# Kernel optimization log

Hardware: AMD Instinct MI355X
Metric: run time of the kernel (lower is better)

Reference implementation:

```python
import jax, jax.numpy as jnp
import numpy as np

TOP_K = 2
SCALING = 32.0 / 64.0  # lora_alpha / reservoir_size


def setup_inputs() -> dict:
    key = jax.random.key(0)
    ks = jax.random.split(key, 6)
    Bsz, S, Din, Dout, R, E = 4, 2048, 4096, 4096, 64, 16
    x = jax.random.normal(ks[0], (Bsz, S, Din), dtype=jnp.float32)
    base_w = jax.random.normal(ks[1], (Dout, Din), dtype=jnp.float32) * 0.02
    base_b = jax.random.normal(ks[2], (Dout,), dtype=jnp.float32) * 0.02
    A = jax.random.normal(ks[3], (R, Din), dtype=jnp.float32) * (1.0 / np.sqrt(Din))
    B = jax.random.normal(ks[4], (E, Dout, R), dtype=jnp.float32) * 0.02
    router_w = jax.random.normal(ks[5], (E, Din), dtype=jnp.float32) * 0.02
    return {"x": x, "base_w": base_w, "base_b": base_b, "A": A, "B": B, "router_w": router_w}


def reference(x, base_w, base_b, A, B, router_w):
    # base linear: [b,s,din] @ [dout,din]^T + bias
    base_out = jnp.einsum('bsi,oi->bso', x, base_w) + base_b
    # low-rank projection through fixed reservoir A (activation=identity, dropout off)
    res_hidden = jnp.einsum('bsi,ri->bsr', x, A)          # [b,s,r]
    # routing
    logits = jnp.einsum('bsi,ei->bse', x, router_w)       # [b,s,E]
    probs = jax.nn.softmax(logits, axis=-1)
    topw, topi = jax.lax.top_k(probs, TOP_K)              # [b,s,k]
    topw = topw / (jnp.sum(topw, axis=-1, keepdims=True) + 1e-6)
    num_experts = B.shape[0]
    # combine weights per expert: sum_k w_k * onehot(idx_k)  -> [b,s,E]
    combine = jnp.sum(jax.nn.one_hot(topi, num_experts, dtype=x.dtype) * topw[..., None], axis=-2)
    # weighted per-expert lowrank B matmul and combine
    delta = jnp.einsum('bse,bsr,eor->bso', combine, res_hidden, B)
    return base_out + delta * SCALING
```

## Files before the change

### kernel.cpp

```cpp
#include <hip/hip_runtime.h>
#include <cstdint>
#include <cstddef>

typedef short short8 __attribute__((ext_vector_type(8)));
typedef float f32x4 __attribute__((ext_vector_type(4)));

#define DIN  4096
#define DOUT 4096
#define RANK 64
#define NEXP 16
#define NTOK 8192
#define KCAT 5120
#define NKT  (KCAT / 64)
#define ROWB (KCAT * 2)

__device__ __forceinline__ unsigned short f2bf(float f) {
    unsigned int u = __builtin_bit_cast(unsigned int, f);
    u = (u + 0x7FFFu + ((u >> 16) & 1u)) >> 16;
    return (unsigned short)u;
}
__device__ __forceinline__ void async_cp16(const void* g, void* lds) {
    __builtin_amdgcn_global_load_lds(
        (const __attribute__((address_space(1))) void*)g,
        (__attribute__((address_space(3))) void*)lds, 16, 0, 0);
}

__global__ void __launch_bounds__(256) prep_all_kernel(
        const float* __restrict__ x, const float* __restrict__ rw,
        const float* __restrict__ bw, const float* __restrict__ Bm,
        const float* __restrict__ Am,
        unsigned short* __restrict__ Xcat, unsigned short* __restrict__ Wcat,
        unsigned short* __restrict__ W1A, float* __restrict__ Lg) {
    __shared__ __align__(16) float xsl[8][532];
    __shared__ __align__(16) float red[8][16][16];
    const int tid = threadIdx.x;

    if (blockIdx.x < 1024) {
        const int t0 = blockIdx.x * 8;
        const int tt = tid >> 5, l32 = tid & 31;
        const int eg = tid >> 6, ts = (tid >> 4) & 3, cc = tid & 15;
        float part[2][4] = {};

        for (int w = 0; w < 8; ++w) {
            #pragma unroll
            for (int sub = 0; sub < 4; ++sub) {
                const int col = w * 512 + sub * 128 + l32 * 4;
                const float4 xv = *(const float4*)&x[(size_t)(t0 + tt) * DIN + col];
                unsigned short b0 = f2bf(xv.x), b1 = f2bf(xv.y),
                               b2 = f2bf(xv.z), b3 = f2bf(xv.w);
                uint2 pk = { (unsigned)b0 | ((unsigned)b1 << 16),
                             (unsigned)b2 | ((unsigned)b3 << 16) };
                *(uint2*)&Xcat[(size_t)(t0 + tt) * KCAT + col] = pk;
                *(float4*)&xsl[tt][sub * 128 + l32 * 4] = xv;
            }
            __syncthreads();
            #pragma unroll
            for (int j = 0; j < 8; ++j) {
                const int colb = w * 512 + (j * 16 + cc) * 4;
                const float4 r0 = *(const float4*)&rw[(size_t)(eg * 4 + 0) * DIN + colb];
                const float4 r1 = *(const float4*)&rw[(size_t)(eg * 4 + 1) * DIN + colb];
                const float4 r2 = *(const float4*)&rw[(size_t)(eg * 4 + 2) * DIN + colb];
                const float4 r3 = *(const float4*)&rw[(size_t)(eg * 4 + 3) * DIN + colb];
                #pragma unroll
                for (int t2 = 0; t2 < 2; ++t2) {
                    const int t = ts * 2 + t2;
                    const float4 xv = *(const float4*)&xsl[t][(j * 16 + cc) * 4];
                    part[t2][0] += xv.x * r0.x + xv.y * r0.y + xv.z * r0.z + xv.w * r0.w;
                    part[t2][1] += xv.x * r1.x + xv.y * r1.y + xv.z * r1.z + xv.w * r1.w;
                    part[t2][2] += xv.x * r2.x + xv.y * r2.y + xv.z * r2.z + xv.w * r2.w;
                    part[t2][3] += xv.x * r3.x + xv.y * r3.y + xv.z * r3.z + xv.w * r3.w;
                }
            }
            __syncthreads();
        }
        #pragma unroll
        for (int t2 = 0; t2 < 2; ++t2)
            #pragma unroll
            for (int e = 0; e < 4; ++e)
                red[ts * 2 + t2][eg * 4 + e][cc] = part[t2][e];
        __syncthreads();
        if (tid < 128) {
            const int t = tid >> 4, e = tid & 15;
            float s = 0.f;
            #pragma unroll
            for (int c = 0; c < 16; ++c) s += red[t][e][c];
            Lg[(size_t)(t0 + t) * NEXP + e] = s;
        }
    } else {
        const unsigned NG1 = (unsigned)DOUT * KCAT / 8u;
        const unsigned NGT = NG1 + 64u * DIN / 8u;
        for (unsigned g = (blockIdx.x - 1024) * 256u + tid; g < NGT;
             g += 2048u * 256u) {
            const float* src;
            unsigned short* dst;
            if (g < NG1) {
                unsigned o  = g / 640u;
                unsigned c8 = (g - o * 640u) * 8u;
                dst = Wcat + (size_t)o * KCAT + c8;
                if (c8 < DIN) {
                    src = bw + (size_t)o * DIN + c8;
                } else {
                    unsigned cc2 = c8 - DIN;
                    unsigned e = cc2 >> 6, r = cc2 & 63u;
                    src = Bm + ((size_t)e * DOUT + o) * RANK + r;
                }
            } else {
                unsigned g2 = g - NG1;
                unsigned row = g2 >> 9;
                unsigned c8  = (g2 & 511u) * 8u;
                dst = W1A + (size_t)row * DIN + c8;
                src = Am + (size_t)row * DIN + c8;
            }
            float4 v0 = *(const float4*)(src);
            float4 v1 = *(const float4*)(src + 4);
            uint4 pk;
            pk.x = (unsigned)f2bf(v0.x) | ((unsigned)f2bf(v0.y) << 16);
            pk.y = (unsigned)f2bf(v0.z) | ((unsigned)f2bf(v0.w) << 16);
            pk.z = (unsigned)f2bf(v1.x) | ((unsigned)f2bf(v1.y) << 16);
            pk.w = (unsigned)f2bf(v1.z) | ((unsigned)f2bf(v1.w) << 16);
            *(uint4*)dst = pk;
        }
    }
}

__global__ void __launch_bounds__(256) proj_moe_kernel(
        const unsigned short* __restrict__ Xcat,
        const unsigned short* __restrict__ W1A,
        const float* __restrict__ Lg, unsigned short* __restrict__ XcatW) {
    __shared__ __align__(16) unsigned short Xs[16 * 128];
    __shared__ __align__(16) unsigned short Ws[64 * 128];
    __shared__ __align__(16) float cw[16][16];
    __shared__ __align__(16) float hbuf[16][68];
    const int tid = threadIdx.x;
    const int wave = tid >> 6, lane = tid & 63;
    const int quad = lane >> 4, l16 = lane & 15;
    const int t0 = blockIdx.x * 16;

    const int rX = tid >> 4, cXs = tid & 15;
    const int cX = (cXs & 8) | ((cXs ^ rX) & 7);

    if (tid < 16) {
        float l[16];
        #pragma unroll
        for (int e = 0; e < 16; ++e) l[e] = Lg[(size_t)(t0 + tid) * NEXP + e];
        int i1 = 0; float b1v = l[0];
        #pragma unroll
        for (int e = 1; e < 16; ++e) if (l[e] > b1v) { b1v = l[e]; i1 = e; }
        int i2 = -1; float b2v = -1e30f;
        #pragma unroll
        for (int e = 0; e < 16; ++e) if (e != i1 && l[e] > b2v) { b2v = l[e]; i2 = e; }
        float S = 0.f;
        #pragma unroll
        for (int e = 0; e < 16; ++e) S += expf(l[e] - b1v);
        const float p1 = 1.0f / S;
        const float p2 = expf(b2v - b1v) / S;
        const float d = p1 + p2 + 1e-6f;
        const float c1 = 0.5f * p1 / d;
        const float c2 = 0.5f * p2 / d;
        #pragma unroll
        for (int e = 0; e < 16; ++e)
            cw[tid][e] = (e == i1) ? c1 : (e == i2) ? c2 : 0.0f;
    }

    f32x4 acc = {};
    for (int kt = 0; kt < DIN / 128; ++kt) {
        const int k0 = kt * 128;
        async_cp16(Xcat + (size_t)(t0 + rX) * KCAT + k0 + cX * 8,
                   (char*)Xs + wave * 1024);
        #pragma unroll
        for (int i = 0; i < 4; ++i) {
            const int s = i * 256 + tid;
            const int rW = s >> 4, cWs = s & 15;
            const int cWc = (cWs & 8) | ((cWs ^ rW) & 7);
            async_cp16(W1A + (size_t)rW * DIN + k0 + cWc * 8,
                       (char*)Ws + i * 4096 + wave * 1024);
        }
        __syncthreads();
        #pragma unroll
        for (int kk = 0; kk < 4; ++kk) {
            const int c = kk * 4 + quad;
            const int sa = ((c & 8) | ((c ^ l16) & 7)) << 3;
            const int rb = wave * 16 + l16;
            const int sb = ((c & 8) | ((c ^ rb) & 7)) << 3;
            short8 am = *(const short8*)&Xs[l16 * 128 + sa];
            short8 bn = *(const short8*)&Ws[rb * 128 + sb];
            acc = __builtin_amdgcn_mfma_f32_16x16x32_bf16(am, bn, acc, 0, 0, 0);
        }
        __syncthreads();
    }
    #pragma unroll
    for (int r = 0; r < 4; ++r)
        hbuf[quad * 4 + r][wave * 16 + l16] = acc[r];
    __syncthreads();
    const int t = tid >> 4, e = tid & 15;
    const float c = cw[t][e];
    unsigned short* dst = XcatW + (size_t)(t0 + t) * KCAT + DIN + e * 64;
    #pragma unroll
    for (int r8 = 0; r8 < 8; ++r8) {
        unsigned short o16[8];
        #pragma unroll
        for (int k = 0; k < 8; ++k)
            o16[k] = f2bf(c * hbuf[t][r8 * 8 + k]);
        uint4 pk;
        pk.x = (unsigned)o16[0] | ((unsigned)o16[1] << 16);
        pk.y = (unsigned)o16[2] | ((unsigned)o16[3] << 16);
        pk.z = (unsigned)o16[4] | ((unsigned)o16[5] << 16);
        pk.w = (unsigned)o16[6] | ((unsigned)o16[7] << 16);
        *(uint4*)(dst + r8 * 8) = pk;
    }
}

__global__ void __launch_bounds__(512, 2) gemm_main_kernel(
        const unsigned short* __restrict__ Xcat,
        const unsigned short* __restrict__ Wcat,
        const float* __restrict__ bias, float* __restrict__ out) {
    __shared__ __align__(16) unsigned short As[2][256 * 64];
    __shared__ __align__(16) unsigned short Bs[2][256 * 64];

    const int tid  = threadIdx.x;
    const int wave = tid >> 6, lane = tid & 63;
    const int l16  = lane & 15, quad = lane >> 4, xb = l16 & 7;
    const int wm   = wave >> 2, wn = wave & 3;

    const int bid = blockIdx.x;
    const int swz = (bid & 7) * 64 + (bid >> 3);
    const int bm0 = (swz & 31) * 256;
    const int bn0 = (swz >> 5) * 256;

    const int urr = tid >> 3;
    const int cks = (tid & 7) ^ (urr & 7);
    const unsigned voffG = (unsigned)(urr * KCAT + cks * 8) * 2u;

    const char* gA = (const char*)Xcat + (size_t)bm0 * ROWB + voffG;
    const char* gB = (const char*)Wcat + (size_t)bn0 * ROWB + voffG;
    char* const ldsA  = (char*)&As[0][0];
    char* const ldsB  = (char*)&Bs[0][0];
    char* const ldswA = ldsA + wave * 1024;
    char* const ldswB = ldsB + wave * 1024;

#define STAGE_A(H, TT, BOFF2) { \
    async_cp16(gA + (size_t)((H) * 64) * ROWB + (size_t)(TT) * 128, \
               ldswA + (BOFF2) + (H) * 8192); \
    async_cp16(gA + (size_t)((H) * 64 + 128) * ROWB + (size_t)(TT) * 128, \
               ldswA + (BOFF2) + (H) * 8192 + 16384); }
#define STAGE_B(U, TT, BOFF2) { \
    async_cp16(gB + (size_t)((U) * 128) * ROWB + (size_t)(TT) * 128, \
               ldswB + (BOFF2) + (U) * 16384); \
    async_cp16(gB + (size_t)((U) * 128 + 64) * ROWB + (size_t)(TT) * 128, \
               ldswB + (BOFF2) + (U) * 16384 + 8192); }

    const int kof0 = ((quad)     ^ xb) * 16;
    const int kof1 = ((4 + quad) ^ xb) * 16;
    const char* ldsAw = ldsA + wm * 16384 + l16 * 128;
    const char* ldsBw = ldsB + wn * 8192  + l16 * 128;

    f32x4 acc[8][4] = {};
    short8 bf[8];
    short8 fE[4], fO[4];

#define READ_BF(BOFF2) { \
    _Pragma("unroll") \
    for (int n = 0; n < 4; ++n) { \
        bf[n * 2 + 0] = *(const short8*)(ldsBw + (BOFF2) + n * 2048 + kof0); \
        bf[n * 2 + 1] = *(const short8*)(ldsBw + (BOFF2) + n * 2048 + kof1); \
    } }
#define PREF_A(DST, Q, BOFF2) { \
    _Pragma("unroll") \
    for (int mm = 0; mm < 2; ++mm) { \
        DST[mm * 2 + 0] = *(const short8*)(ldsAw + (BOFF2) + (2 * (Q) + mm) * 2048 + kof0); \
        DST[mm * 2 + 1] = *(const short8*)(ldsAw + (BOFF2) + (2 * (Q) + mm) * 2048 + kof1); \
    } }
#define MFMA16(AF, Q) { \
    __builtin_amdgcn_s_setprio(1); \
    _Pragma("unroll") \
    for (int kk = 0; kk < 2; ++kk) \
        _Pragma("unroll") \
        for (int mm = 0; mm < 2; ++mm) \
            _Pragma("unroll") \
            for (int n = 0; n < 4; ++n) \
                acc[2 * (Q) + mm][n] = __builtin_amdgcn_mfma_f32_16x16x32_bf16( \
                    AF[mm * 2 + kk], bf[n * 2 + kk], acc[2 * (Q) + mm][n], 0, 0, 0); \
    __builtin_amdgcn_s_setprio(0); }
#define CLOB asm volatile("" ::: "memory")
#define BAR  __builtin_amdgcn_s_barrier()
#define LGKM0 { asm volatile("s_waitcnt lgkmcnt(0)" ::: "memory"); \
                __builtin_amdgcn_sched_barrier(0); }
#define SBAR __builtin_amdgcn_sched_barrier(0)

    STAGE_B(0, 0, 0);     STAGE_B(1, 0, 0);
    STAGE_A(0, 0, 0);     STAGE_A(1, 0, 0);
    STAGE_B(0, 1, 32768); STAGE_B(1, 1, 32768);
    STAGE_A(0, 1, 32768);
    asm volatile("s_waitcnt vmcnt(6)" ::: "memory");
    CLOB; BAR; CLOB;
    PREF_A(fE, 0, 0);

    #pragma unroll 2
    for (int t = 0; t < NKT; ++t) {
        const int boff = (t & 1) * 32768;
        const int ob   = boff ^ 32768;
        const int ts1  = (t + 1 < NKT) ? t + 1 : t;
        const int ts2  = (t + 2 < NKT) ? t + 2 : t;

        READ_BF(boff);
        STAGE_A(1, ts1, ob);
        CLOB; BAR;
        LGKM0;
        PREF_A(fO, 1, boff); SBAR;
        MFMA16(fE, 0);
        SBAR; CLOB; BAR;

        STAGE_B(0, ts2, boff);
        CLOB; BAR;
        LGKM0;
        PREF_A(fE, 2, boff); SBAR;
        MFMA16(fO, 1);
        SBAR; CLOB; BAR;

        STAGE_B(1, ts2, boff);
        CLOB; BAR;
        LGKM0;
        PREF_A(fO, 3, boff); SBAR;
        MFMA16(fE, 2);
        SBAR; CLOB; BAR;

        STAGE_A(0, ts2, boff);
        CLOB; BAR;
        LGKM0;
        asm volatile("s_waitcnt vmcnt(6)" ::: "memory");
        PREF_A(fE, 0, ob); SBAR;
        MFMA16(fO, 3);
        SBAR; CLOB; BAR;
    }

    const int orow = bm0 + wm * 128 + quad * 4;
    #pragma unroll
    for (int n = 0; n < 4; ++n) {
        const int col = bn0 + wn * 64 + n * 16 + l16;
        const float bj = bias[col];
        #pragma unroll
        for (int m = 0; m < 8; ++m)
            #pragma unroll
            for (int r = 0; r < 4; ++r)
                out[(size_t)(orow + m * 16 + r) * DOUT + col] = acc[m][n][r] + bj;
    }
#undef STAGE_A
#undef STAGE_B
#undef READ_BF
#undef PREF_A
#undef MFMA16
#undef CLOB
#undef BAR
#undef LGKM0
#undef SBAR
}

extern "C" void kernel_launch(void* const* d_in, const int* in_sizes, int n_in,
                              void* d_out, int out_size, void* d_ws, size_t ws_size,
                              hipStream_t stream) {
    const float* x  = (const float*)d_in[0];
    const float* bw = (const float*)d_in[1];
    const float* bb = (const float*)d_in[2];
    const float* Am = (const float*)d_in[3];
    const float* Bm = (const float*)d_in[4];
    const float* rw = (const float*)d_in[5];
    float* out = (float*)d_out;
    char* ws = (char*)d_ws;
    unsigned short* Xcat = (unsigned short*)(ws);
    unsigned short* Wcat = (unsigned short*)(ws + 83886080);
    unsigned short* W1A  = (unsigned short*)(ws + 125829120);
    float* Lg = (float*)(ws + 126353408);

    hipLaunchKernelGGL(prep_all_kernel, dim3(3072),   dim3(256), 0, stream,
                       x, rw, bw, Bm, Am, Xcat, Wcat, W1A, Lg);
    hipLaunchKernelGGL(proj_moe_kernel, dim3(512),    dim3(256), 0, stream,
                       Xcat, W1A, Lg, Xcat);
    hipLaunchKernelGGL(gemm_main_kernel, dim3(512),   dim3(512), 0, stream,
                       Xcat, Wcat, bb, out);
}
```

Measured before the change: 667.5 us.

## Double-buffer projection loads and restructure prep kernel work split

The projection kernel now double-buffers its LDS tiles, issuing async global-to-LDS copies for the next K tile before computing on the current one, using explicit vmcnt waits and raw barriers instead of __syncthreads. The prep kernel drops the LDS staging of x and its per-iteration barriers, reading x directly from global for the router logits. The A-matrix conversion moves into the token blocks, and the weight-conversion blocks use a fixed two-rows-per-block mapping instead of a grid-stride loop. The intent is to overlap memory latency with MFMA work and remove synchronisation in prep. The cost is doubled LDS use and redundant global reads of x, which rely on cache hits.

```diff
diff --git a/kernel.cpp b/kernel.cpp
--- a/kernel.cpp
+++ b/kernel.cpp
@@ -31,29 +31,48 @@
         const float* __restrict__ Am,
         unsigned short* __restrict__ Xcat, unsigned short* __restrict__ Wcat,
         unsigned short* __restrict__ W1A, float* __restrict__ Lg) {
-    __shared__ __align__(16) float xsl[8][532];
-    __shared__ __align__(16) float red[8][16][16];
     const int tid = threadIdx.x;
 
     if (blockIdx.x < 1024) {
+        __shared__ __align__(16) float red[8][16][16];
         const int t0 = blockIdx.x * 8;
+
         const int tt = tid >> 5, l32 = tid & 31;
-        const int eg = tid >> 6, ts = (tid >> 4) & 3, cc = tid & 15;
-        float part[2][4] = {};
-
+        const float* xrow = x + (size_t)(t0 + tt) * DIN;
+        unsigned short* xcrow = Xcat + (size_t)(t0 + tt) * KCAT;
+        #pragma unroll
         for (int w = 0; w < 8; ++w) {
             #pragma unroll
             for (int sub = 0; sub < 4; ++sub) {
                 const int col = w * 512 + sub * 128 + l32 * 4;
-                const float4 xv = *(const float4*)&x[(size_t)(t0 + tt) * DIN + col];
-                unsigned short b0 = f2bf(xv.x), b1 = f2bf(xv.y),
-                               b2 = f2bf(xv.z), b3 = f2bf(xv.w);
-                uint2 pk = { (unsigned)b0 | ((unsigned)b1 << 16),
-                             (unsigned)b2 | ((unsigned)b3 << 16) };
-                *(uint2*)&Xcat[(size_t)(t0 + tt) * KCAT + col] = pk;
-                *(float4*)&xsl[tt][sub * 128 + l32 * 4] = xv;
+                const float4 xv = *(const float4*)&xrow[col];
+                uint2 pk = { (unsigned)f2bf(xv.x) | ((unsigned)f2bf(xv.y) << 16),
+                             (unsigned)f2bf(xv.z) | ((unsigned)f2bf(xv.w) << 16) };
+                *(uint2*)&xcrow[col] = pk;
             }
-            __syncthreads();
+        }
+
+        if (tid < 32) {
+            const unsigned g2 = (unsigned)blockIdx.x * 32u + (unsigned)tid;
+            const unsigned row = g2 >> 9;
+            const unsigned c8  = (g2 & 511u) * 8u;
+            const float* src = Am + (size_t)row * DIN + c8;
+            unsigned short* dst = W1A + (size_t)row * DIN + c8;
+            float4 v0 = *(const float4*)(src);
+            float4 v1 = *(const float4*)(src + 4);
+            uint4 pk;
+            pk.x = (unsigned)f2bf(v0.x) | ((unsigned)f2bf(v0.y) << 16);
+            pk.y = (unsigned)f2bf(v0.z) | ((unsigned)f2bf(v0.w) << 16);
+            pk.z = (unsigned)f2bf(v1.x) | ((unsigned)f2bf(v1.y) << 16);
+            pk.w = (unsigned)f2bf(v1.z) | ((unsigned)f2bf(v1.w) << 16);
+            *(uint4*)dst = pk;
+        }
+
+        const int eg = tid >> 6, ts = (tid >> 4) & 3, cc = tid & 15;
+        const float* xt0 = x + (size_t)(t0 + ts * 2 + 0) * DIN;
+        const float* xt1 = x + (size_t)(t0 + ts * 2 + 1) * DIN;
+        float part[2][4] = {};
+        for (int w = 0; w < 8; ++w) {
             #pragma unroll
             for (int j = 0; j < 8; ++j) {
                 const int colb = w * 512 + (j * 16 + cc) * 4;
@@ -61,17 +80,17 @@
                 const float4 r1 = *(const float4*)&rw[(size_t)(eg * 4 + 1) * DIN + colb];
                 const float4 r2 = *(const float4*)&rw[(size_t)(eg * 4 + 2) * DIN + colb];
                 const float4 r3 = *(const float4*)&rw[(size_t)(eg * 4 + 3) * DIN + colb];
-                #pragma unroll
-                for (int t2 = 0; t2 < 2; ++t2) {
-                    const int t = ts * 2 + t2;
-                    const float4 xv = *(const float4*)&xsl[t][(j * 16 + cc) * 4];
-                    part[t2][0] += xv.x * r0.x + xv.y * r0.y + xv.z * r0.z + xv.w * r0.w;
-                    part[t2][1] += xv.x * r1.x + xv.y * r1.y + xv.z * r1.z + xv.w * r1.w;
-                    part[t2][2] += xv.x * r2.x + xv.y * r2.y + xv.z * r2.z + xv.w * r2.w;
-                    part[t2][3] += xv.x * r3.x + xv.y * r3.y + xv.z * r3.z + xv.w * r3.w;
-                }
+                const float4 xv0 = *(const float4*)&xt0[colb];
+                const float4 xv1 = *(const float4*)&xt1[colb];
+                part[0][0] += xv0.x * r0.x + xv0.y * r0.y + xv0.z * r0.z + xv0.w * r0.w;
+                part[0][1] += xv0.x * r1.x + xv0.y * r1.y + xv0.z * r1.z + xv0.w * r1.w;
+                part[0][2] += xv0.x * r2.x + xv0.y * r2.y + xv0.z * r2.z + xv0.w * r2.w;
+                part[0][3] += xv0.x * r3.x + xv0.y * r3.y + xv0.z * r3.z + xv0.w * r3.w;
+                part[1][0] += xv1.x * r0.x + xv1.y * r0.y + xv1.z * r0.z + xv1.w * r0.w;
+                part[1][1] += xv1.x * r1.x + xv1.y * r1.y + xv1.z * r1.z + xv1.w * r1.w;
+                part[1][2] += xv1.x * r2.x + xv1.y * r2.y + xv1.z * r2.z + xv1.w * r2.w;
+                part[1][3] += xv1.x * r3.x + xv1.y * r3.y + xv1.z * r3.z + xv1.w * r3.w;
             }
-            __syncthreads();
         }
         #pragma unroll
         for (int t2 = 0; t2 < 2; ++t2)
@@ -87,29 +106,19 @@
             Lg[(size_t)(t0 + t) * NEXP + e] = s;
         }
     } else {
-        const unsigned NG1 = (unsigned)DOUT * KCAT / 8u;
-        const unsigned NGT = NG1 + 64u * DIN / 8u;
-        for (unsigned g = (blockIdx.x - 1024) * 256u + tid; g < NGT;
-             g += 2048u * 256u) {
+        const int b = blockIdx.x - 1024;
+        #pragma unroll
+        for (int i = 0; i < 5; ++i) {
+            const int g  = tid + i * 256;
+            const int r2 = (g >= 640) ? 1 : 0;
+            const int o  = 2 * b + r2;
+            const int c8 = (g - r2 * 640) * 8;
             const float* src;
-            unsigned short* dst;
-            if (g < NG1) {
-                unsigned o  = g / 640u;
-                unsigned c8 = (g - o * 640u) * 8u;
-                dst = Wcat + (size_t)o * KCAT + c8;
-                if (c8 < DIN) {
-                    src = bw + (size_t)o * DIN + c8;
-                } else {
-                    unsigned cc2 = c8 - DIN;
-                    unsigned e = cc2 >> 6, r = cc2 & 63u;
-                    src = Bm + ((size_t)e * DOUT + o) * RANK + r;
-                }
+            if (c8 < DIN) {
+                src = bw + (size_t)o * DIN + c8;
             } else {
-                unsigned g2 = g - NG1;
-                unsigned row = g2 >> 9;
-                unsigned c8  = (g2 & 511u) * 8u;
-                dst = W1A + (size_t)row * DIN + c8;
-                src = Am + (size_t)row * DIN + c8;
+                const int cc2 = c8 - DIN;
+                src = Bm + ((size_t)(cc2 >> 6) * DOUT + o) * RANK + (cc2 & 63);
             }
             float4 v0 = *(const float4*)(src);
             float4 v1 = *(const float4*)(src + 4);
@@ -118,7 +127,7 @@
             pk.y = (unsigned)f2bf(v0.z) | ((unsigned)f2bf(v0.w) << 16);
             pk.z = (unsigned)f2bf(v1.x) | ((unsigned)f2bf(v1.y) << 16);
             pk.w = (unsigned)f2bf(v1.z) | ((unsigned)f2bf(v1.w) << 16);
-            *(uint4*)dst = pk;
+            *(uint4*)&Wcat[(size_t)o * KCAT + c8] = pk;
         }
     }
 }
@@ -127,8 +136,8 @@
         const unsigned short* __restrict__ Xcat,
         const unsigned short* __restrict__ W1A,
         const float* __restrict__ Lg, unsigned short* __restrict__ XcatW) {
-    __shared__ __align__(16) unsigned short Xs[16 * 128];
-    __shared__ __align__(16) unsigned short Ws[64 * 128];
+    __shared__ __align__(16) unsigned short Xs[2][16 * 128];
+    __shared__ __align__(16) unsigned short Ws[2][64 * 128];
     __shared__ __align__(16) float cw[16][16];
     __shared__ __align__(16) float hbuf[16][68];
     const int tid = threadIdx.x;
@@ -161,33 +170,50 @@
         for (int e = 0; e < 16; ++e)
             cw[tid][e] = (e == i1) ? c1 : (e == i2) ? c2 : 0.0f;
     }
+    asm volatile("s_waitcnt vmcnt(0) lgkmcnt(0)" ::: "memory");
+
+    const unsigned short* srcX = Xcat + (size_t)(t0 + rX) * KCAT + cX * 8;
+    const unsigned short* srcW[4];
+    int ldsWo[4];
+    #pragma unroll
+    for (int i = 0; i < 4; ++i) {
+        const int s = i * 256 + tid;
+        const int rW = s >> 4, cWs = s & 15;
+        const int cWc = (cWs & 8) | ((cWs ^ rW) & 7);
+        srcW[i] = W1A + (size_t)rW * DIN + cWc * 8;
+        ldsWo[i] = i * 4096 + wave * 1024;
+    }
+#define STAGE_K(D, KT) { \
+    async_cp16(srcX + (size_t)(KT) * 128, (char*)&Xs[D][0] + wave * 1024); \
+    _Pragma("unroll") \
+    for (int i = 0; i < 4; ++i) \
+        async_cp16(srcW[i] + (size_t)(KT) * 128, (char*)&Ws[D][0] + ldsWo[i]); }
 
     f32x4 acc = {};
+    STAGE_K(0, 0);
     for (int kt = 0; kt < DIN / 128; ++kt) {
-        const int k0 = kt * 128;
-        async_cp16(Xcat + (size_t)(t0 + rX) * KCAT + k0 + cX * 8,
-                   (char*)Xs + wave * 1024);
-        #pragma unroll
-        for (int i = 0; i < 4; ++i) {
-            const int s = i * 256 + tid;
-            const int rW = s >> 4, cWs = s & 15;
-            const int cWc = (cWs & 8) | ((cWs ^ rW) & 7);
-            async_cp16(W1A + (size_t)rW * DIN + k0 + cWc * 8,
-                       (char*)Ws + i * 4096 + wave * 1024);
-        }
-        __syncthreads();
+        const int d = kt & 1;
+        if (kt < DIN / 128 - 1) {
+            STAGE_K(d ^ 1, kt + 1);
+            asm volatile("s_waitcnt vmcnt(5)" ::: "memory");
+        } else {
+            asm volatile("s_waitcnt vmcnt(0)" ::: "memory");
+        }
+        __builtin_amdgcn_s_barrier();
         #pragma unroll
         for (int kk = 0; kk < 4; ++kk) {
             const int c = kk * 4 + quad;
             const int sa = ((c & 8) | ((c ^ l16) & 7)) << 3;
             const int rb = wave * 16 + l16;
             const int sb = ((c & 8) | ((c ^ rb) & 7)) << 3;
-            short8 am = *(const short8*)&Xs[l16 * 128 + sa];
-            short8 bn = *(const short8*)&Ws[rb * 128 + sb];
+            short8 am = *(const short8*)&Xs[d][l16 * 128 + sa];
+            short8 bn = *(const short8*)&Ws[d][rb * 128 + sb];
             acc = __builtin_amdgcn_mfma_f32_16x16x32_bf16(am, bn, acc, 0, 0, 0);
         }
-        __syncthreads();
-    }
+        asm volatile("s_waitcnt lgkmcnt(0)" ::: "memory");
+        __builtin_amdgcn_s_barrier();
+    }
+#undef STAGE_K
     #pragma unroll
     for (int r = 0; r < 4; ++r)
         hbuf[quad * 4 + r][wave * 16 + l16] = acc[r];
```

Result: slower. 710.9 us (+6.5%).
